# Optimization experiments

Hardware: AMD Instinct MI355X
Metric: run time of the kernel (lower is better)

Reference implementation:

```python
import jax, jax.numpy as jnp
import numpy as np
from jax import lax

H1, H2, H3, T, IN = 15, 60, 20, 15, 1


def lstm_layer(x, W_ih, W_hh, b_ih, b_hh):
    # x: [B, T, in] -> hs: [B, T, H]; PyTorch gate order i, f, g, o
    B = x.shape[0]
    H = W_hh.shape[1]
    h0 = jnp.zeros((B, H), x.dtype)
    c0 = jnp.zeros((B, H), x.dtype)
    b = b_ih + b_hh

    def step(carry, xt):
        h, c = carry
        g = xt @ W_ih.T + h @ W_hh.T + b  # [B, 4H]
        i, f, gg, o = jnp.split(g, 4, axis=-1)
        i = jax.nn.sigmoid(i)
        f = jax.nn.sigmoid(f)
        gg = jnp.tanh(gg)
        o = jax.nn.sigmoid(o)
        c = f * c + i * gg
        h = o * jnp.tanh(c)
        return (h, c), h

    _, hs = lax.scan(step, (h0, c0), jnp.swapaxes(x, 0, 1))  # hs: [T, B, H]
    return jnp.swapaxes(hs, 0, 1)


def setup_inputs() -> dict:
    key = jax.random.key(0)
    ks = jax.random.split(key, 16)
    s = 0.1
    B = 131072
    inp = {
        "x": jax.random.normal(ks[0], (B, T, IN), jnp.float32),
        "W_ih0": jax.random.normal(ks[1], (4 * H1, IN), jnp.float32) * s,
        "W_hh0": jax.random.normal(ks[2], (4 * H1, H1), jnp.float32) * s,
        "b_ih0": jax.random.normal(ks[3], (4 * H1,), jnp.float32) * s,
        "b_hh0": jax.random.normal(ks[4], (4 * H1,), jnp.float32) * s,
        "W_ih1": jax.random.normal(ks[5], (4 * H1, H1), jnp.float32) * s,
        "W_hh1": jax.random.normal(ks[6], (4 * H1, H1), jnp.float32) * s,
        "b_ih1": jax.random.normal(ks[7], (4 * H1,), jnp.float32) * s,
        "b_hh1": jax.random.normal(ks[8], (4 * H1,), jnp.float32) * s,
        "W1": jax.random.normal(ks[9], (H2, H1), jnp.float32) * s,
        "b1": jax.random.normal(ks[10], (H2,), jnp.float32) * s,
        "W2": jax.random.normal(ks[11], (H3, H2), jnp.float32) * s,
        "b2": jax.random.normal(ks[12], (H3,), jnp.float32) * s,
        "W3": jax.random.normal(ks[13], (1, H3), jnp.float32) * s,
        "b3": jax.random.normal(ks[14], (1,), jnp.float32) * s,
    }
    return inp


def reference(x, W_ih0, W_hh0, b_ih0, b_hh0, W_ih1, W_hh1, b_ih1, b_hh1, W1, b1, W2, b2, W3, b3):
    h1 = lstm_layer(x, W_ih0, W_hh0, b_ih0, b_hh0)   # [B, T, H1]
    h2 = lstm_layer(h1, W_ih1, W_hh1, b_ih1, b_hh1)  # [B, T, H1] (eval mode: no dropout)
    feat = h2[:, :, -1]                              # [B, T] == [B, 15]
    out1 = feat @ W1.T + b1                          # [B, 60]
    out2 = out1 @ W2.T + b2                          # [B, 20]
    out = out2 @ W3.T + b3                           # [B, 1]
    return out
```

## Files before the change

### kernel.cpp

```cpp
#include <hip/hip_runtime.h>

#define HH   15
#define TT   15
#define NH2  60
#define NH3  20

#define LOG2E 1.44269504088896340736f
#define L2E2  2.88539008177792680736f

typedef _Float16 f16x8 __attribute__((ext_vector_type(8)));
typedef float    f32x4 __attribute__((ext_vector_type(4)));

#define WS_V  2048
#define WS_CB 2063

__device__ __forceinline__ float fast_rcp(float x)  { return __builtin_amdgcn_rcpf(x); }
__device__ __forceinline__ float fast_exp2(float x) { return __builtin_amdgcn_exp2f(x); }
__device__ __forceinline__ float sigm_s(float y) { return fast_rcp(1.0f + fast_exp2(-y)); }
__device__ __forceinline__ float tanh_s(float y) { return 1.0f - 2.0f * fast_rcp(1.0f + fast_exp2(y)); }

__global__ void lstm_prep(const float* __restrict__ Wih0, const float* __restrict__ Whh0,
                          const float* __restrict__ bih0, const float* __restrict__ bhh0,
                          const float* __restrict__ Wih1, const float* __restrict__ Whh1,
                          const float* __restrict__ bih1, const float* __restrict__ bhh1,
                          const float* __restrict__ W1, const float* __restrict__ b1,
                          const float* __restrict__ W2, const float* __restrict__ b2,
                          const float* __restrict__ W3, const float* __restrict__ b3,
                          float* __restrict__ wsf)
{
    const int tid = threadIdx.x;
    unsigned* wsu = (unsigned*)wsf;

    {
        const int f = tid >> 6, l = tid & 63;
        const int n = f & 3;
        const bool isL2 = (f >= 4);
        const int u = l & 15, g = l >> 4;
        const float sc = (n == 2) ? L2E2 : LOG2E;
        const int r = n * 15 + u;
        float vals[8];
        #pragma unroll
        for (int j = 0; j < 8; ++j) {
            const int k = g * 8 + j;
            float v = 0.0f;
            if (u < 15) {
                if (!isL2) {
                    if (k < 15)       v = Whh0[r * 15 + k];
                    else if (k == 15) v = Wih0[r];
                    else if (k == 16) v = bih0[r] + bhh0[r];
                } else {
                    if (k < 15)       v = Wih1[r * 15 + k];
                    else if (k == 15) v = bih1[r] + bhh1[r];
                    else if (k < 31)  v = Whh1[r * 15 + (k - 16)];
                }
            }
            vals[j] = v * sc;
        }
        #pragma unroll
        for (int d = 0; d < 4; ++d) {
            union { _Float16 h[2]; unsigned u32; } p;
            p.h[0] = (_Float16)vals[2 * d];
            p.h[1] = (_Float16)vals[2 * d + 1];
            wsu[f * 256 + l * 4 + d] = p.u32;
        }
    }

    __shared__ float sU[NH2];
    if (tid < NH2) {
        float ua = 0.0f;
        #pragma unroll
        for (int k = 0; k < NH3; ++k) ua = fmaf(W3[k], W2[k * NH2 + tid], ua);
        sU[tid] = ua;
    }
    __syncthreads();
    if (tid < TT) {
        float v = 0.0f;
        for (int j = 0; j < NH2; ++j) v = fmaf(sU[j], W1[j * HH + tid], v);
        wsf[WS_V + tid] = v;
    }
    if (tid == 0) {
        float c = b3[0];
        for (int k = 0; k < NH3; ++k) c = fmaf(W3[k], b2[k], c);
        for (int j = 0; j < NH2; ++j) c = fmaf(sU[j], b1[j], c);
        wsf[WS_CB] = c;
    }
}

__global__ __launch_bounds__(256)
__attribute__((amdgpu_waves_per_eu(4)))
void lstm_mfma(const float* __restrict__ x, const float* __restrict__ wsf,
               float* __restrict__ out, int B)
{
    const int tid = threadIdx.x;
    const int wid = tid >> 6;
    const int l   = tid & 63;
    const int u   = l & 15;
    const int g   = l >> 4;
    const int wbase = (blockIdx.x * 4 + wid) * 16;

    __shared__ __align__(16) _Float16 lds[4][2][16][32];

    unsigned* ldsw = (unsigned*)&lds[wid][0][0][0];
    #pragma unroll
    for (int i = 0; i < 8; ++i) ldsw[l + 64 * i] = 0u;
    if (l < 16) {
        lds[wid][0][l][16] = (_Float16)1.0f;
        lds[wid][1][l][15] = (_Float16)1.0f;
    }

    const uint4* wsq = (const uint4*)wsf;
    union FU { uint4 q; f16x8 h; };
#define LOADB(name, fidx) f16x8 name; { FU t_; t_.q = wsq[(fidx) * 64 + l]; name = t_.h; }
    LOADB(B0, 0) LOADB(B1, 1) LOADB(B2, 2) LOADB(B3, 3)
    LOADB(B4, 4) LOADB(B5, 5) LOADB(B6, 6) LOADB(B7, 7)
#undef LOADB

    const float cb = wsf[WS_CB];
    f32x4 acc = {cb, cb, cb, cb};
    f32x4 c1  = {0.0f, 0.0f, 0.0f, 0.0f};
    f32x4 c2  = {0.0f, 0.0f, 0.0f, 0.0f};
    const f32x4 zc = {0.0f, 0.0f, 0.0f, 0.0f};

    const float* xrow = x + (size_t)(wbase + u) * TT;

#define MFMA(a, b, c) __builtin_amdgcn_mfma_f32_16x16x32_f16((a), (b), (c), 0, 0, 0)

    #pragma unroll 1
    for (int t = 0; t < TT; ++t) {
        if (l < 16) lds[wid][0][l][15] = (_Float16)xrow[t];

        const f16x8 a1 = *(const f16x8*)&lds[wid][0][u][g * 8];
        f32x4 d0 = MFMA(a1, B0, zc);
        f32x4 d1 = MFMA(a1, B1, zc);
        f32x4 d2 = MFMA(a1, B2, zc);
        f32x4 d3 = MFMA(a1, B3, zc);

#define UPD1(i) { \
        const float si = sigm_s(d0[i]); \
        const float sf = sigm_s(d1[i]); \
        const float tg = tanh_s(d2[i]); \
        const float so = sigm_s(d3[i]); \
        const float cc = fmaf(si, tg, sf * c1[i]); \
        c1[i] = cc; \
        const float hh = so * tanh_s(L2E2 * cc); \
        const _Float16 hf = (_Float16)hh; \
        lds[wid][0][4 * g + (i)][u] = hf; \
        if (u < 15) lds[wid][1][4 * g + (i)][u] = hf; }
        UPD1(0) UPD1(1) UPD1(2) UPD1(3)
#undef UPD1

        const f16x8 a2 = *(const f16x8*)&lds[wid][1][u][g * 8];
        d0 = MFMA(a2, B4, zc);
        d1 = MFMA(a2, B5, zc);
        d2 = MFMA(a2, B6, zc);
        d3 = MFMA(a2, B7, zc);

        const float vt = wsf[WS_V + t];
#define UPD2(i) { \
        const float si = sigm_s(d0[i]); \
        const float sf = sigm_s(d1[i]); \
        const float tg = tanh_s(d2[i]); \
        const float so = sigm_s(d3[i]); \
        const float cc = fmaf(si, tg, sf * c2[i]); \
        c2[i] = cc; \
        const float hh = so * tanh_s(L2E2 * cc); \
        lds[wid][1][4 * g + (i)][16 + u] = (_Float16)hh; \
        acc[i] = fmaf(hh, vt, acc[i]); }
        UPD2(0) UPD2(1) UPD2(2) UPD2(3)
#undef UPD2
    }
#undef MFMA

    if (u == 14) {
        out[wbase + 4 * g + 0] = acc[0];
        out[wbase + 4 * g + 1] = acc[1];
        out[wbase + 4 * g + 2] = acc[2];
        out[wbase + 4 * g + 3] = acc[3];
    }
}

extern "C" void kernel_launch(void* const* d_in, const int* in_sizes, int n_in,
                              void* d_out, int out_size, void* d_ws, size_t ws_size,
                              hipStream_t stream) {
    (void)n_in; (void)ws_size; (void)out_size;
    const float* x    = (const float*)d_in[0];
    const float* Wih0 = (const float*)d_in[1];
    const float* Whh0 = (const float*)d_in[2];
    const float* bih0 = (const float*)d_in[3];
    const float* bhh0 = (const float*)d_in[4];
    const float* Wih1 = (const float*)d_in[5];
    const float* Whh1 = (const float*)d_in[6];
    const float* bih1 = (const float*)d_in[7];
    const float* bhh1 = (const float*)d_in[8];
    const float* W1   = (const float*)d_in[9];
    const float* b1   = (const float*)d_in[10];
    const float* W2   = (const float*)d_in[11];
    const float* b2   = (const float*)d_in[12];
    const float* W3   = (const float*)d_in[13];
    const float* b3   = (const float*)d_in[14];
    float* out = (float*)d_out;
    float* wsf = (float*)d_ws;

    const int B = in_sizes[0] / TT;

    lstm_prep<<<1, 512, 0, stream>>>(Wih0, Whh0, bih0, bhh0,
                                     Wih1, Whh1, bih1, bhh1,
                                     W1, b1, W2, b2, W3, b3, wsf);

    const int grid = B / (16 * 4);
    lstm_mfma<<<grid, 256, 0, stream>>>(x, wsf, out, B);
}
```

Measured before the change: 144.8 us.

## Fuse weight-prep kernel into LSTM kernel and merge gate reciprocals

Removes the separate single-block prep kernel and has every block build its fp16 MFMA weight fragments and collapsed head vector in shared memory. This drops one launch and the serialization between the two kernels. The cost is redundant per-block prep work and extra barriers. The gate math is also rewritten so that sigmoid(i)*tanh(g) and sigmoid(o)*tanh(c) each share one reciprocal, cutting rcp ops per step. The LDS row padding changes from 32 to 40 and the waves_per_eu hint is dropped.

```diff
diff --git a/kernel.cpp b/kernel.cpp
--- a/kernel.cpp
+++ b/kernel.cpp
@@ -11,86 +11,25 @@
 typedef _Float16 f16x8 __attribute__((ext_vector_type(8)));
 typedef float    f32x4 __attribute__((ext_vector_type(4)));
 
-#define WS_V  2048
-#define WS_CB 2063
-
 __device__ __forceinline__ float fast_rcp(float x)  { return __builtin_amdgcn_rcpf(x); }
 __device__ __forceinline__ float fast_exp2(float x) { return __builtin_amdgcn_exp2f(x); }
-__device__ __forceinline__ float sigm_s(float y) { return fast_rcp(1.0f + fast_exp2(-y)); }
-__device__ __forceinline__ float tanh_s(float y) { return 1.0f - 2.0f * fast_rcp(1.0f + fast_exp2(y)); }
-
-__global__ void lstm_prep(const float* __restrict__ Wih0, const float* __restrict__ Whh0,
-                          const float* __restrict__ bih0, const float* __restrict__ bhh0,
-                          const float* __restrict__ Wih1, const float* __restrict__ Whh1,
-                          const float* __restrict__ bih1, const float* __restrict__ bhh1,
-                          const float* __restrict__ W1, const float* __restrict__ b1,
-                          const float* __restrict__ W2, const float* __restrict__ b2,
-                          const float* __restrict__ W3, const float* __restrict__ b3,
-                          float* __restrict__ wsf)
-{
-    const int tid = threadIdx.x;
-    unsigned* wsu = (unsigned*)wsf;
-
-    {
-        const int f = tid >> 6, l = tid & 63;
-        const int n = f & 3;
-        const bool isL2 = (f >= 4);
-        const int u = l & 15, g = l >> 4;
-        const float sc = (n == 2) ? L2E2 : LOG2E;
-        const int r = n * 15 + u;
-        float vals[8];
-        #pragma unroll
-        for (int j = 0; j < 8; ++j) {
-            const int k = g * 8 + j;
-            float v = 0.0f;
-            if (u < 15) {
-                if (!isL2) {
-                    if (k < 15)       v = Whh0[r * 15 + k];
-                    else if (k == 15) v = Wih0[r];
-                    else if (k == 16) v = bih0[r] + bhh0[r];
-                } else {
-                    if (k < 15)       v = Wih1[r * 15 + k];
-                    else if (k == 15) v = bih1[r] + bhh1[r];
-                    else if (k < 31)  v = Whh1[r * 15 + (k - 16)];
-                }
-            }
-            vals[j] = v * sc;
-        }
-        #pragma unroll
-        for (int d = 0; d < 4; ++d) {
-            union { _Float16 h[2]; unsigned u32; } p;
-            p.h[0] = (_Float16)vals[2 * d];
-            p.h[1] = (_Float16)vals[2 * d + 1];
-            wsu[f * 256 + l * 4 + d] = p.u32;
-        }
-    }
-
-    __shared__ float sU[NH2];
-    if (tid < NH2) {
-        float ua = 0.0f;
-        #pragma unroll
-        for (int k = 0; k < NH3; ++k) ua = fmaf(W3[k], W2[k * NH2 + tid], ua);
-        sU[tid] = ua;
-    }
-    __syncthreads();
-    if (tid < TT) {
-        float v = 0.0f;
-        for (int j = 0; j < NH2; ++j) v = fmaf(sU[j], W1[j * HH + tid], v);
-        wsf[WS_V + tid] = v;
-    }
-    if (tid == 0) {
-        float c = b3[0];
-        for (int k = 0; k < NH3; ++k) c = fmaf(W3[k], b2[k], c);
-        for (int j = 0; j < NH2; ++j) c = fmaf(sU[j], b1[j], c);
-        wsf[WS_CB] = c;
-    }
-}
 
 __global__ __launch_bounds__(256)
-__attribute__((amdgpu_waves_per_eu(4)))
-void lstm_mfma(const float* __restrict__ x, const float* __restrict__ wsf,
+void lstm_mfma(const float* __restrict__ x,
+               const float* __restrict__ Wih0, const float* __restrict__ Whh0,
+               const float* __restrict__ bih0, const float* __restrict__ bhh0,
+               const float* __restrict__ Wih1, const float* __restrict__ Whh1,
+               const float* __restrict__ bih1, const float* __restrict__ bhh1,
+               const float* __restrict__ W1, const float* __restrict__ b1,
+               const float* __restrict__ W2, const float* __restrict__ b2,
+               const float* __restrict__ W3, const float* __restrict__ b3,
                float* __restrict__ out, int B)
 {
+    __shared__ __align__(16) _Float16 lds[4][2][16][40];
+    __shared__ __align__(16) uint4 fragLDS[8][64];
+    __shared__ float sU[NH2];
+    __shared__ float sHead[16];
+
     const int tid = threadIdx.x;
     const int wid = tid >> 6;
     const int l   = tid & 63;
@@ -98,24 +37,92 @@
     const int g   = l >> 4;
     const int wbase = (blockIdx.x * 4 + wid) * 16;
 
-    __shared__ __align__(16) _Float16 lds[4][2][16][32];
-
-    unsigned* ldsw = (unsigned*)&lds[wid][0][0][0];
-    #pragma unroll
-    for (int i = 0; i < 8; ++i) ldsw[l + 64 * i] = 0u;
+    if (tid < NH2) {
+        float ua = 0.0f;
+        #pragma unroll
+        for (int k = 0; k < NH3; ++k) ua = fmaf(W3[k], W2[k * NH2 + tid], ua);
+        sU[tid] = ua;
+    }
+
+    {
+        const int f = tid >> 6, ll = tid & 63;
+        const int n = f;
+        const int uu = ll & 15, gg = ll >> 4;
+        const float sc = (n == 2) ? L2E2 : LOG2E;
+        const int rr = n * 15 + (uu < 15 ? uu : 0);
+        const float wx = Wih0[rr];
+        const float bb = bih0[rr] + bhh0[rr];
+        union { uint4 q; _Float16 h[8]; } pk;
+        #pragma unroll
+        for (int j = 0; j < 8; ++j) {
+            const int k = gg * 8 + j;
+            const int kc = (k < 15) ? k : 0;
+            float v = Whh0[rr * 15 + kc];
+            if (k == 15) v = wx;
+            if (k == 16) v = bb;
+            if (k > 16)  v = 0.0f;
+            pk.h[j] = (_Float16)((uu < 15) ? v * sc : 0.0f);
+        }
+        fragLDS[f][ll] = pk.q;
+    }
+    {
+        const int f = 4 + (tid >> 6), ll = tid & 63;
+        const int n = f & 3;
+        const int uu = ll & 15, gg = ll >> 4;
+        const float sc = (n == 2) ? L2E2 : LOG2E;
+        const int rr = n * 15 + (uu < 15 ? uu : 0);
+        const float bb = bih1[rr] + bhh1[rr];
+        union { uint4 q; _Float16 h[8]; } pk;
+        #pragma unroll
+        for (int j = 0; j < 8; ++j) {
+            const int k = gg * 8 + j;
+            const int k1 = (k < 15) ? k : 0;
+            const int k2 = (k >= 16 && k < 31) ? (k - 16) : 0;
+            const float vA = Wih1[rr * 15 + k1];
+            const float vC = Whh1[rr * 15 + k2];
+            float v = (k < 15) ? vA : ((k == 15) ? bb : ((k < 31) ? vC : 0.0f));
+            pk.h[j] = (_Float16)((uu < 15) ? v * sc : 0.0f);
+        }
+        fragLDS[f][ll] = pk.q;
+    }
+
+    {
+        unsigned* zw = (unsigned*)&lds[wid][0][0][0];
+        #pragma unroll
+        for (int i = 0; i < 10; ++i) zw[l + 64 * i] = 0u;
+    }
+
+    __syncthreads();
+
+    if (tid < TT) {
+        float v = 0.0f;
+        #pragma unroll
+        for (int j = 0; j < NH2; ++j) v = fmaf(sU[j], W1[j * HH + tid], v);
+        sHead[tid] = v;
+    }
+    if (tid == 0) {
+        float c = b3[0];
+        #pragma unroll
+        for (int k = 0; k < NH3; ++k) c = fmaf(W3[k], b2[k], c);
+        #pragma unroll
+        for (int j = 0; j < NH2; ++j) c = fmaf(sU[j], b1[j], c);
+        sHead[15] = c;
+    }
+
+    union FU { uint4 q; f16x8 h; };
+#define LOADB(name, fidx) f16x8 name; { FU t_; t_.q = fragLDS[fidx][l]; name = t_.h; }
+    LOADB(B0, 0) LOADB(B1, 1) LOADB(B2, 2) LOADB(B3, 3)
+    LOADB(B4, 4) LOADB(B5, 5) LOADB(B6, 6) LOADB(B7, 7)
+#undef LOADB
+
     if (l < 16) {
         lds[wid][0][l][16] = (_Float16)1.0f;
         lds[wid][1][l][15] = (_Float16)1.0f;
     }
 
-    const uint4* wsq = (const uint4*)wsf;
-    union FU { uint4 q; f16x8 h; };
-#define LOADB(name, fidx) f16x8 name; { FU t_; t_.q = wsq[(fidx) * 64 + l]; name = t_.h; }
-    LOADB(B0, 0) LOADB(B1, 1) LOADB(B2, 2) LOADB(B3, 3)
-    LOADB(B4, 4) LOADB(B5, 5) LOADB(B6, 6) LOADB(B7, 7)
-#undef LOADB
-
-    const float cb = wsf[WS_CB];
+    __syncthreads();
+
+    const float cb = sHead[15];
     f32x4 acc = {cb, cb, cb, cb};
     f32x4 c1  = {0.0f, 0.0f, 0.0f, 0.0f};
     f32x4 c2  = {0.0f, 0.0f, 0.0f, 0.0f};
@@ -136,13 +143,15 @@
         f32x4 d3 = MFMA(a1, B3, zc);
 
 #define UPD1(i) { \
-        const float si = sigm_s(d0[i]); \
-        const float sf = sigm_s(d1[i]); \
-        const float tg = tanh_s(d2[i]); \
-        const float so = sigm_s(d3[i]); \
-        const float cc = fmaf(si, tg, sf * c1[i]); \
+        const float ei = fast_exp2(-d0[i]); \
+        const float ef = fast_exp2(-d1[i]); \
+        const float eg = fast_exp2(d2[i]); \
+        const float eo = fast_exp2(-d3[i]); \
+        const float itg = (eg - 1.0f) * fast_rcp((1.0f + ei) * (eg + 1.0f)); \
+        const float cc = fmaf(fast_rcp(1.0f + ef), c1[i], itg); \
         c1[i] = cc; \
-        const float hh = so * tanh_s(L2E2 * cc); \
+        const float ec = fast_exp2(L2E2 * cc); \
+        const float hh = (ec - 1.0f) * fast_rcp((1.0f + eo) * (ec + 1.0f)); \
         const _Float16 hf = (_Float16)hh; \
         lds[wid][0][4 * g + (i)][u] = hf; \
         if (u < 15) lds[wid][1][4 * g + (i)][u] = hf; }
@@ -155,15 +164,17 @@
         d2 = MFMA(a2, B6, zc);
         d3 = MFMA(a2, B7, zc);
 
-        const float vt = wsf[WS_V + t];
+        const float vt = sHead[t];
 #define UPD2(i) { \
-        const float si = sigm_s(d0[i]); \
-        const float sf = sigm_s(d1[i]); \
-        const float tg = tanh_s(d2[i]); \
-        const float so = sigm_s(d3[i]); \
-        const float cc = fmaf(si, tg, sf * c2[i]); \
+        const float ei = fast_exp2(-d0[i]); \
+        const float ef = fast_exp2(-d1[i]); \
+        const float eg = fast_exp2(d2[i]); \
+        const float eo = fast_exp2(-d3[i]); \
+        const float itg = (eg - 1.0f) * fast_rcp((1.0f + ei) * (eg + 1.0f)); \
+        const float cc = fmaf(fast_rcp(1.0f + ef), c2[i], itg); \
         c2[i] = cc; \
-        const float hh = so * tanh_s(L2E2 * cc); \
+        const float ec = fast_exp2(L2E2 * cc); \
+        const float hh = (ec - 1.0f) * fast_rcp((1.0f + eo) * (ec + 1.0f)); \
         lds[wid][1][4 * g + (i)][16 + u] = (_Float16)hh; \
         acc[i] = fmaf(hh, vt, acc[i]); }
         UPD2(0) UPD2(1) UPD2(2) UPD2(3)
@@ -182,7 +193,7 @@
 extern "C" void kernel_launch(void* const* d_in, const int* in_sizes, int n_in,
                               void* d_out, int out_size, void* d_ws, size_t ws_size,
                               hipStream_t stream) {
-    (void)n_in; (void)ws_size; (void)out_size;
+    (void)n_in; (void)d_ws; (void)ws_size; (void)out_size;
     const float* x    = (const float*)d_in[0];
     const float* Wih0 = (const float*)d_in[1];
     const float* Whh0 = (const float*)d_in[2];
@@ -199,14 +210,11 @@
     const float* W3   = (const float*)d_in[13];
     const float* b3   = (const float*)d_in[14];
     float* out = (float*)d_out;
-    float* wsf = (float*)d_ws;
 
     const int B = in_sizes[0] / TT;
 
-    lstm_prep<<<1, 512, 0, stream>>>(Wih0, Whh0, bih0, bhh0,
-                                     Wih1, Whh1, bih1, bhh1,
-                                     W1, b1, W2, b2, W3, b3, wsf);
-
     const int grid = B / (16 * 4);
-    lstm_mfma<<<grid, 256, 0, stream>>>(x, wsf, out, B);
+    lstm_mfma<<<grid, 256, 0, stream>>>(x, Wih0, Whh0, bih0, bhh0,
+                                        Wih1, Whh1, bih1, bhh1,
+                                        W1, b1, W2, b2, W3, b3, out, B);
 }
```

After: 149.4 us. 1.03x slower.

## Software-pipeline the two LSTM layers and fuse gate reciprocals

Applied to the files above, without the earlier changes.

Restructures the time loop so the layer-1 MFMAs for step t+1 are issued before the layer-2 gate update of step t, letting the two layers' work overlap. Gate math is reworked so the sigmoid of the input gate and the tanh of the candidate (and likewise the output gate and tanh(c)) share a single reciprocal, reducing transcendental instructions. It also pads the LDS rows to 40 halfs to reduce bank conflicts, redirects lane 15's write to a dummy column instead of branching, and drops the waves_per_eu hint. The combined formulas can overflow for large pre-activations, and register pressure may rise without the occupancy hint.

```diff
diff --git a/kernel.cpp b/kernel.cpp
--- a/kernel.cpp
+++ b/kernel.cpp
@@ -16,8 +16,6 @@
 
 __device__ __forceinline__ float fast_rcp(float x)  { return __builtin_amdgcn_rcpf(x); }
 __device__ __forceinline__ float fast_exp2(float x) { return __builtin_amdgcn_exp2f(x); }
-__device__ __forceinline__ float sigm_s(float y) { return fast_rcp(1.0f + fast_exp2(-y)); }
-__device__ __forceinline__ float tanh_s(float y) { return 1.0f - 2.0f * fast_rcp(1.0f + fast_exp2(y)); }
 
 __global__ void lstm_prep(const float* __restrict__ Wih0, const float* __restrict__ Whh0,
                           const float* __restrict__ bih0, const float* __restrict__ bhh0,
@@ -37,7 +35,7 @@
         const bool isL2 = (f >= 4);
         const int u = l & 15, g = l >> 4;
         const float sc = (n == 2) ? L2E2 : LOG2E;
-        const int r = n * 15 + u;
+        const int r = n * 15 + (u < 15 ? u : 0);
         float vals[8];
         #pragma unroll
         for (int j = 0; j < 8; ++j) {
@@ -87,10 +85,11 @@
 }
 
 __global__ __launch_bounds__(256)
-__attribute__((amdgpu_waves_per_eu(4)))
 void lstm_mfma(const float* __restrict__ x, const float* __restrict__ wsf,
                float* __restrict__ out, int B)
 {
+    __shared__ __align__(16) _Float16 lds[4][2][16][40];
+
     const int tid = threadIdx.x;
     const int wid = tid >> 6;
     const int l   = tid & 63;
@@ -98,14 +97,10 @@
     const int g   = l >> 4;
     const int wbase = (blockIdx.x * 4 + wid) * 16;
 
-    __shared__ __align__(16) _Float16 lds[4][2][16][32];
-
-    unsigned* ldsw = (unsigned*)&lds[wid][0][0][0];
-    #pragma unroll
-    for (int i = 0; i < 8; ++i) ldsw[l + 64 * i] = 0u;
-    if (l < 16) {
-        lds[wid][0][l][16] = (_Float16)1.0f;
-        lds[wid][1][l][15] = (_Float16)1.0f;
+    {
+        unsigned* zw = (unsigned*)&lds[wid][0][0][0];
+        #pragma unroll
+        for (int i = 0; i < 10; ++i) zw[l + 64 * i] = 0u;
     }
 
     const uint4* wsq = (const uint4*)wsf;
@@ -115,6 +110,13 @@
     LOADB(B4, 4) LOADB(B5, 5) LOADB(B6, 6) LOADB(B7, 7)
 #undef LOADB
 
+    if (l < 16) {
+        lds[wid][0][l][16] = (_Float16)1.0f;
+        lds[wid][1][l][15] = (_Float16)1.0f;
+    }
+
+    const int u1col = (u == 15) ? 31 : u;
+
     const float cb = wsf[WS_CB];
     f32x4 acc = {cb, cb, cb, cb};
     f32x4 c1  = {0.0f, 0.0f, 0.0f, 0.0f};
@@ -125,50 +127,73 @@
 
 #define MFMA(a, b, c) __builtin_amdgcn_mfma_f32_16x16x32_f16((a), (b), (c), 0, 0, 0)
 
-    #pragma unroll 1
-    for (int t = 0; t < TT; ++t) {
-        if (l < 16) lds[wid][0][l][15] = (_Float16)xrow[t];
-
-        const f16x8 a1 = *(const f16x8*)&lds[wid][0][u][g * 8];
-        f32x4 d0 = MFMA(a1, B0, zc);
-        f32x4 d1 = MFMA(a1, B1, zc);
-        f32x4 d2 = MFMA(a1, B2, zc);
-        f32x4 d3 = MFMA(a1, B3, zc);
-
 #define UPD1(i) { \
-        const float si = sigm_s(d0[i]); \
-        const float sf = sigm_s(d1[i]); \
-        const float tg = tanh_s(d2[i]); \
-        const float so = sigm_s(d3[i]); \
-        const float cc = fmaf(si, tg, sf * c1[i]); \
+        const float ei = fast_exp2(-d0[i]); \
+        const float ef = fast_exp2(-d1[i]); \
+        const float eg = fast_exp2(d2[i]); \
+        const float eo = fast_exp2(-d3[i]); \
+        const float itg = (eg - 1.0f) * fast_rcp((1.0f + ei) * (eg + 1.0f)); \
+        const float cc = fmaf(fast_rcp(1.0f + ef), c1[i], itg); \
         c1[i] = cc; \
-        const float hh = so * tanh_s(L2E2 * cc); \
+        const float ec = fast_exp2(L2E2 * cc); \
+        const float hh = (ec - 1.0f) * fast_rcp((1.0f + eo) * (ec + 1.0f)); \
         const _Float16 hf = (_Float16)hh; \
         lds[wid][0][4 * g + (i)][u] = hf; \
-        if (u < 15) lds[wid][1][4 * g + (i)][u] = hf; }
-        UPD1(0) UPD1(1) UPD1(2) UPD1(3)
-#undef UPD1
-
-        const f16x8 a2 = *(const f16x8*)&lds[wid][1][u][g * 8];
-        d0 = MFMA(a2, B4, zc);
-        d1 = MFMA(a2, B5, zc);
-        d2 = MFMA(a2, B6, zc);
-        d3 = MFMA(a2, B7, zc);
-
-        const float vt = wsf[WS_V + t];
+        lds[wid][1][4 * g + (i)][u1col] = hf; }
+
 #define UPD2(i) { \
-        const float si = sigm_s(d0[i]); \
-        const float sf = sigm_s(d1[i]); \
-        const float tg = tanh_s(d2[i]); \
-        const float so = sigm_s(d3[i]); \
-        const float cc = fmaf(si, tg, sf * c2[i]); \
+        const float ei = fast_exp2(-e0[i]); \
+        const float ef = fast_exp2(-e1[i]); \
+        const float eg = fast_exp2(e2[i]); \
+        const float eo = fast_exp2(-e3[i]); \
+        const float itg = (eg - 1.0f) * fast_rcp((1.0f + ei) * (eg + 1.0f)); \
+        const float cc = fmaf(fast_rcp(1.0f + ef), c2[i], itg); \
         c2[i] = cc; \
-        const float hh = so * tanh_s(L2E2 * cc); \
+        const float ec = fast_exp2(L2E2 * cc); \
+        const float hh = (ec - 1.0f) * fast_rcp((1.0f + eo) * (ec + 1.0f)); \
         lds[wid][1][4 * g + (i)][16 + u] = (_Float16)hh; \
         acc[i] = fmaf(hh, vt, acc[i]); }
+
+    if (l < 16) lds[wid][0][l][15] = (_Float16)xrow[0];
+    f16x8 a1 = *(const f16x8*)&lds[wid][0][u][g * 8];
+    f32x4 d0 = MFMA(a1, B0, zc);
+    f32x4 d1 = MFMA(a1, B1, zc);
+    f32x4 d2 = MFMA(a1, B2, zc);
+    f32x4 d3 = MFMA(a1, B3, zc);
+
+    #pragma unroll 2
+    for (int t = 0; t < TT - 1; ++t) {
+        UPD1(0) UPD1(1) UPD1(2) UPD1(3)
+
+        const f16x8 a2 = *(const f16x8*)&lds[wid][1][u][g * 8];
+        f32x4 e0 = MFMA(a2, B4, zc);
+        f32x4 e1 = MFMA(a2, B5, zc);
+        f32x4 e2 = MFMA(a2, B6, zc);
+        f32x4 e3 = MFMA(a2, B7, zc);
+
+        if (l < 16) lds[wid][0][l][15] = (_Float16)xrow[t + 1];
+        a1 = *(const f16x8*)&lds[wid][0][u][g * 8];
+        d0 = MFMA(a1, B0, zc);
+        d1 = MFMA(a1, B1, zc);
+        d2 = MFMA(a1, B2, zc);
+        d3 = MFMA(a1, B3, zc);
+
+        const float vt = wsf[WS_V + t];
         UPD2(0) UPD2(1) UPD2(2) UPD2(3)
+    }
+
+    {
+        UPD1(0) UPD1(1) UPD1(2) UPD1(3)
+        const f16x8 a2 = *(const f16x8*)&lds[wid][1][u][g * 8];
+        f32x4 e0 = MFMA(a2, B4, zc);
+        f32x4 e1 = MFMA(a2, B5, zc);
+        f32x4 e2 = MFMA(a2, B6, zc);
+        f32x4 e3 = MFMA(a2, B7, zc);
+        const float vt = wsf[WS_V + (TT - 1)];
+        UPD2(0) UPD2(1) UPD2(2) UPD2(3)
+    }
+#undef UPD1
 #undef UPD2
-    }
 #undef MFMA
 
     if (u == 14) {
```

Measured after the change: 145.7 us. Within noise of the previous version (+0.6%).
